# Performance work log

Hardware: AMD Instinct MI355X
Metric: run time of the kernel (lower is better)

The kernel has to match this reference:

```python
import jax, jax.numpy as jnp
import numpy as np

T, K = 131072, 128  # turns, num_tags


def setup_inputs() -> dict:
    key = jax.random.key(0)
    ks = jax.random.split(key, 8)
    emissions = jax.random.normal(ks[0], (T, K), dtype=jnp.float32)
    tags = jax.random.randint(ks[1], (T,), 0, K)
    who2who = jax.random.randint(ks[2], (T - 1,), 0, 2)
    init_count = jax.random.randint(ks[3], (T - 1,), 0, 2)
    distance = jax.random.randint(ks[4], (T - 1,), 0, 3)
    class_weights = jax.random.uniform(ks[5], (K,), jnp.float32, 0.5, 1.5)
    # DistanceCRF transition matrices stacked: [s2u, u2s_n0, u2s_n1_d2, u2s_n1_dgt2]
    trans_stack = jax.random.normal(ks[6], (4, K, K), dtype=jnp.float32) * 0.1
    start_scores = jax.random.normal(ks[7], (K,), dtype=jnp.float32) * 0.1
    return {
        "emissions": emissions,
        "trans_stack": trans_stack,
        "start_scores": start_scores,
        "class_weights": class_weights,
        "tags": tags,
        "who2who": who2who,
        "init_count": init_count,
        "distance": distance,
    }


def _trans_idx(who2who, init_count, distance):
    # DistanceCRF decision tree from _get_trans:
    #   w==1 -> s2u (0); init_count==0 -> u2s_n0 (1);
    #   distance==0 -> u2s_n1_d2 (2); else -> u2s_n1_dgt2 (3)
    return jnp.where(
        who2who == 1, 0,
        jnp.where(init_count == 0, 1, jnp.where(distance == 0, 2, 3)),
    )


def reference(emissions, trans_stack, start_scores, class_weights,
              tags, who2who, init_count, distance):
    idx = _trans_idx(who2who, init_count, distance)  # [T-1]

    # ---- gold path score (fully vectorized) ----
    w = class_weights[tags]                                   # [T]
    em_gold = jnp.take_along_axis(emissions, tags[:, None], axis=1)[:, 0]  # [T]
    tr_gold = trans_stack[idx, tags[:-1], tags[1:]]           # [T-1]
    gold = w[0] * (start_scores[tags[0]] + em_gold[0]) \
        + jnp.sum(w[1:] * (tr_gold + em_gold[1:]))

    # ---- forward algorithm (log partition) ----
    def step(alphas, xs):
        i, em_t = xs
        tr = trans_stack[i]                                   # [K,K] gathered per step
        scores = alphas[:, None] + tr + em_t[None, :]         # [K,K]
        return jax.nn.logsumexp(scores, axis=0), None

    alpha0 = start_scores + emissions[0]
    alphas, _ = jax.lax.scan(step, alpha0, (idx, emissions[1:]))
    log_Z = jax.nn.logsumexp(alphas)
    return gold, log_Z
```

## Files before the change

kernel.cpp:

```cpp
#include <hip/hip_runtime.h>

#define T_LEN 131072
#define KDIM 128
#define CHUNK 32
#define WARM 16
#define NSTEP (CHUNK + WARM)
#define NCHUNK (T_LEN / CHUNK)
#define GROUPC 16
#define NGRP (NCHUNK / GROUPC)
#define CSHIFT 4.5f

typedef float v4f __attribute__((ext_vector_type(4)));
typedef short s8v __attribute__((ext_vector_type(8)));

__device__ __forceinline__ int trans_idx(int w2w, int ic, int dist) {
    return (w2w == 1) ? 0 : (ic == 0 ? 1 : (dist == 0 ? 2 : 3));
}
__device__ __forceinline__ unsigned short bf16rne(float x) {
    unsigned u = __float_as_uint(x);
    return (unsigned short)((u + 0x7fffu + ((u >> 16) & 1u)) >> 16);
}
__device__ __forceinline__ float bf16tof(unsigned short h) {
    return __uint_as_float(((unsigned)h) << 16);
}

__global__ void __launch_bounds__(512, 1) scan_kernel(
    const float* __restrict__ em, const float* __restrict__ trans,
    const float* __restrict__ start, const float* __restrict__ cw,
    const int* __restrict__ tags, const int* __restrict__ w2w,
    const int* __restrict__ ic, const int* __restrict__ dist,
    double* __restrict__ goldslots, double* __restrict__ logzslots,
    unsigned* __restrict__ donecnt, float* __restrict__ out)
{
    const int tid = threadIdx.x;
    const int wv  = tid >> 6;
    const int mh  = wv >> 2;
    const int wvc = wv & 3;
    const int ln  = tid & 63;
    const int lr  = ln & 15;
    const int hq  = ln >> 4;
    const int grp = blockIdx.x;

    __shared__ float SS[32][130];
    __shared__ __align__(16) unsigned short A[2][GROUPC * KDIM];
    __shared__ double bg[8];
    __shared__ double bzred;
    __shared__ double redd[256];
    __shared__ int islast;

    s8v Bf[2][2][4];
    const int ncol = (wvc << 5) + lr;
    {
        const int sr = tid >> 4;
        const int sc = (tid & 15) << 3;
        float4 nx0, nx1;
        {
            const float* s = trans + (tid << 3);
            nx0 = *(const float4*)(s); nx1 = *(const float4*)(s + 4);
        }
        #pragma unroll
        for (int p = 0; p < 16; ++p) {
            ((float2*)&SS[sr][sc])[0] = make_float2(nx0.x, nx0.y);
            ((float2*)&SS[sr][sc])[1] = make_float2(nx0.z, nx0.w);
            ((float2*)&SS[sr][sc + 4])[0] = make_float2(nx1.x, nx1.y);
            ((float2*)&SS[sr][sc + 4])[1] = make_float2(nx1.z, nx1.w);
            __syncthreads();
            if (p < 15) {
                const float* s = trans + ((p + 1) << 12) + (tid << 3);
                nx0 = *(const float4*)(s); nx1 = *(const float4*)(s + 4);
            }
            if ((p >> 3) == mh) {
                const int mloc = (p >> 2) & 1, ks = p & 3;
                s8v f0, f1;
                #pragma unroll
                for (int j = 0; j < 8; ++j) {
                    f0[j] = (short)bf16rne(__expf(SS[(hq << 3) + j][ncol]));
                    f1[j] = (short)bf16rne(__expf(SS[(hq << 3) + j][ncol + 16]));
                }
                Bf[mloc][0][ks] = f0;
                Bf[mloc][1][ks] = f1;
            }
            __syncthreads();
        }
    }

    {
        float gp = 0.f;
        const int t = 1 + (grp << 9) + tid;
        if (t < T_LEN) {
            const int tg  = tags[t];
            const int tgp = tags[t - 1];
            const int mm  = trans_idx(w2w[t - 1], ic[t - 1], dist[t - 1]);
            gp = cw[tg] * (trans[((size_t)mm * KDIM + tgp) * KDIM + tg] +
                           em[(size_t)t * KDIM + tg]);
        }
        if (grp == 0 && tid == 0) {
            const int tg0 = tags[0];
            gp += cw[tg0] * (start[tg0] + em[tg0]);
        }
        float r = gp;
        #pragma unroll
        for (int off = 32; off; off >>= 1) r += __shfl_down(r, off, 64);
        if (ln == 0) bg[wv] = (double)r;
    }

    if (wv == 0) {
        const int c_row = (grp << 4) + lr;
        #pragma unroll
        for (int kk = 0; kk < 32; kk += 2) {
            const int k = (hq << 5) + kk;
            float a0, a1;
            if (c_row == 0) {
                a0 = __expf(start[k] + em[k]);
                a1 = __expf(start[k + 1] + em[k + 1]);
            } else { a0 = 1.f; a1 = 1.f; }
            const int off = (lr << 8) + ((k << 1) ^ ((lr & 7) << 4));
            *(unsigned*)((char*)A[0] + off) =
                (unsigned)bf16rne(a0) | ((unsigned)bf16rne(a1) << 16);
        }
    }
    __syncthreads();

    int t0r[4];
    #pragma unroll
    for (int r = 0; r < 4; ++r) {
        const int c_r = (grp << 4) + (hq << 2) + r;
        t0r[r] = (c_r == 0) ? 1 : (1 + c_r * CHUNK - WARM);
    }
    const int c_lr   = (grp << 4) + lr;
    const int town_l = 1 + c_lr * CHUNK;
    const int tend_l = min(town_l + CHUNK, T_LEN);
    const int t0_l   = (c_lr == 0) ? 1 : (town_l - WARM);

    int pmw, pmi, pmd;
    {
        const int ix = min(t0_l - 1, T_LEN - 2);
        pmw = w2w[ix]; pmi = ic[ix]; pmd = dist[ix];
    }
    float pem[2][4];
    #pragma unroll
    for (int r = 0; r < 4; ++r) {
        const int t = min(t0r[r], T_LEN - 1);
        pem[0][r] = em[(size_t)t * KDIM + ncol];
        pem[1][r] = em[(size_t)t * KDIM + ncol + 16];
    }

    float g = 0.f;
    float sc4[4] = {1.f, 1.f, 1.f, 1.f};

    for (int it = 0; it <= NSTEP; ++it) {
        s8v Af[4];
        #pragma unroll
        for (int ks = 0; ks < 4; ++ks) {
            const int off = (lr << 8) + (((ks << 6) + (hq << 4)) ^ ((lr & 7) << 4));
            Af[ks] = *(const s8v*)((const char*)A[it & 1] + off);
        }

        const bool trig = ((it & 7) == 0) || (grp == NGRP - 1 && it == NSTEP - 1);
        if (trig) {
            float s = 0.f;
            #pragma unroll
            for (int ks = 0; ks < 4; ++ks) {
                #pragma unroll
                for (int j = 0; j < 8; ++j)
                    s += bf16tof((unsigned short)Af[ks][j]);
            }
            s += __shfl_xor(s, 16, 64);
            s += __shfl_xor(s, 32, 64);
            const int tprev = t0_l + it - 1;
            const bool dn = ((tprev & 7) == 0) || (tprev == T_LEN - 1);
            const float scl = dn ? (1.f / s) : 1.f;
            if (it == 0) {
                if (c_lr == 0) g += __logf(s);
            } else if (dn && tprev >= town_l && tprev < tend_l) {
                g += __logf(s);
            }
            #pragma unroll
            for (int r = 0; r < 4; ++r) sc4[r] = __shfl(scl, (hq << 2) + r, 64);
        }
        if (it == NSTEP) break;

        const int mcur = trans_idx(pmw, pmi, pmd);
        int m4[4];
        #pragma unroll
        for (int r = 0; r < 4; ++r) m4[r] = __shfl(mcur, (hq << 2) + r, 64);
        float dv[2][4];
        #pragma unroll
        for (int nt = 0; nt < 2; ++nt) {
            #pragma unroll
            for (int r = 0; r < 4; ++r)
                dv[nt][r] = __expf(pem[nt][r] - CSHIFT) * sc4[r];
        }

        {
            const int ix = min(t0_l + it, T_LEN - 2);
            pmw = w2w[ix]; pmi = ic[ix]; pmd = dist[ix];
        }
        #pragma unroll
        for (int r = 0; r < 4; ++r) {
            const int t = min(t0r[r] + it + 1, T_LEN - 1);
            pem[0][r] = em[(size_t)t * KDIM + ncol];
            pem[1][r] = em[(size_t)t * KDIM + ncol + 16];
        }

        v4f acc[2][2];
        #pragma unroll
        for (int m = 0; m < 2; ++m) {
            #pragma unroll
            for (int nt = 0; nt < 2; ++nt) acc[m][nt] = (v4f)0.f;
        }
        #pragma unroll
        for (int ks = 0; ks < 4; ++ks) {
            #pragma unroll
            for (int m = 0; m < 2; ++m) {
                #pragma unroll
                for (int nt = 0; nt < 2; ++nt)
                    acc[m][nt] = __builtin_amdgcn_mfma_f32_16x16x32_bf16(
                        Af[ks], Bf[m][nt][ks], acc[m][nt], 0, 0, 0);
            }
        }

        #pragma unroll
        for (int nt = 0; nt < 2; ++nt) {
            #pragma unroll
            for (int r = 0; r < 4; ++r) {
                const int mm = m4[r];
                if ((mm >> 1) == mh) {
                    const float y = ((mm & 1) ? acc[1][nt][r] : acc[0][nt][r])
                                    * dv[nt][r];
                    const int row = (hq << 2) + r;
                    const int col = (wvc << 5) + (nt << 4) + lr;
                    const int off = (row << 8) + ((col << 1) ^ ((row & 7) << 4));
                    *(unsigned short*)((char*)A[(it & 1) ^ 1] + off) = bf16rne(y);
                }
            }
        }
        #pragma unroll
        for (int r = 0; r < 4; ++r) sc4[r] = 1.f;
        __syncthreads();
    }

    if (wv == 0) {
        float gz = (ln < 16) ? (g + CSHIFT * (float)(tend_l - town_l)) : 0.f;
        float r = gz;
        #pragma unroll
        for (int off = 32; off; off >>= 1) r += __shfl_down(r, off, 64);
        if (ln == 0) bzred = (double)r;
    }
    __syncthreads();

    if (tid == 0) {
        goldslots[grp] = bg[0] + bg[1] + bg[2] + bg[3] +
                         bg[4] + bg[5] + bg[6] + bg[7];
        logzslots[grp] = bzred;
        __threadfence();
        const unsigned prev = atomicAdd(donecnt, 1u);
        islast = (prev == NGRP - 1) ? 1 : 0;
    }
    __syncthreads();
    if (islast) {
        __threadfence();
        if (tid < 256) redd[tid] = goldslots[tid];
        __syncthreads();
        for (int s = 128; s > 0; s >>= 1) {
            if (tid < s && tid < 256) redd[tid] += redd[tid + s];
            __syncthreads();
        }
        if (tid == 0) out[0] = (float)redd[0];
        __syncthreads();
        if (tid < 256) redd[tid] = logzslots[tid];
        __syncthreads();
        for (int s = 128; s > 0; s >>= 1) {
            if (tid < s && tid < 256) redd[tid] += redd[tid + s];
            __syncthreads();
        }
        if (tid == 0) out[1] = (float)redd[0];
    }
}

extern "C" void kernel_launch(void* const* d_in, const int* in_sizes, int n_in,
                              void* d_out, int out_size, void* d_ws, size_t ws_size,
                              hipStream_t stream) {
    const float* emissions = (const float*)d_in[0];
    const float* trans     = (const float*)d_in[1];
    const float* start     = (const float*)d_in[2];
    const float* cw        = (const float*)d_in[3];
    const int*   tags      = (const int*)d_in[4];
    const int*   w2w       = (const int*)d_in[5];
    const int*   icnt      = (const int*)d_in[6];
    const int*   dist      = (const int*)d_in[7];

    double*   goldslots = (double*)d_ws;
    double*   logzslots = (double*)d_ws + 256;
    unsigned* donecnt   = (unsigned*)((double*)d_ws + 512);

    hipMemsetAsync(donecnt, 0, sizeof(unsigned), stream);
    scan_kernel<<<NGRP, 512, 0, stream>>>(emissions, trans, start, cw, tags,
                                          w2w, icnt, dist, goldslots, logzslots,
                                          donecnt, (float*)d_out);
}
```

Before: 170.7 us.

## Halve chunk length and double chunks per block with 1024-thread blocks

Cuts the per-chunk sequential scan from 32 to 16 owned steps, which shortens the serial critical path from 48 to 32 steps including warm-up. Each block now holds 32 chunks as two 16-row MFMA tiles using 16 waves, so the grid stays at 256 blocks. The per-step __syncthreads is replaced with an explicit lgkmcnt wait plus s_barrier. In exchange, warm-up work rises relative to useful work, 1024-thread blocks put more register pressure on each CU, and shorter warm-up chunks may be less accurate.

```diff
diff --git a/kernel.cpp b/kernel.cpp
--- a/kernel.cpp
+++ b/kernel.cpp
@@ -2,11 +2,11 @@
 
 #define T_LEN 131072
 #define KDIM 128
-#define CHUNK 32
+#define CHUNK 16
 #define WARM 16
 #define NSTEP (CHUNK + WARM)
 #define NCHUNK (T_LEN / CHUNK)
-#define GROUPC 16
+#define GROUPC 32
 #define NGRP (NCHUNK / GROUPC)
 #define CSHIFT 4.5f
 
@@ -24,7 +24,7 @@
     return __uint_as_float(((unsigned)h) << 16);
 }
 
-__global__ void __launch_bounds__(512, 1) scan_kernel(
+__global__ void __launch_bounds__(1024) scan_kernel(
     const float* __restrict__ em, const float* __restrict__ trans,
     const float* __restrict__ start, const float* __restrict__ cw,
     const int* __restrict__ tags, const int* __restrict__ w2w,
@@ -32,42 +32,37 @@
     double* __restrict__ goldslots, double* __restrict__ logzslots,
     unsigned* __restrict__ donecnt, float* __restrict__ out)
 {
-    const int tid = threadIdx.x;
-    const int wv  = tid >> 6;
-    const int mh  = wv >> 2;
-    const int wvc = wv & 3;
-    const int ln  = tid & 63;
-    const int lr  = ln & 15;
-    const int hq  = ln >> 4;
-    const int grp = blockIdx.x;
+    const int tid  = threadIdx.x;
+    const int wv   = tid >> 6;
+    const int mrow = wv >> 3;
+    const int mh   = (wv >> 2) & 1;
+    const int wvc  = wv & 3;
+    const int ln   = tid & 63;
+    const int lr   = ln & 15;
+    const int hq   = ln >> 4;
+    const int grp  = blockIdx.x;
 
     __shared__ float SS[32][130];
     __shared__ __align__(16) unsigned short A[2][GROUPC * KDIM];
-    __shared__ double bg[8];
-    __shared__ double bzred;
+    __shared__ double bg[16];
+    __shared__ double bzred[2];
     __shared__ double redd[256];
     __shared__ int islast;
 
     s8v Bf[2][2][4];
     const int ncol = (wvc << 5) + lr;
     {
-        const int sr = tid >> 4;
-        const int sc = (tid & 15) << 3;
-        float4 nx0, nx1;
-        {
-            const float* s = trans + (tid << 3);
-            nx0 = *(const float4*)(s); nx1 = *(const float4*)(s + 4);
-        }
+        const int sr = tid >> 5;
+        const int sc = (tid & 31) << 2;
+        float4 nx;
+        nx = *(const float4*)(trans + (tid << 2));
         #pragma unroll
         for (int p = 0; p < 16; ++p) {
-            ((float2*)&SS[sr][sc])[0] = make_float2(nx0.x, nx0.y);
-            ((float2*)&SS[sr][sc])[1] = make_float2(nx0.z, nx0.w);
-            ((float2*)&SS[sr][sc + 4])[0] = make_float2(nx1.x, nx1.y);
-            ((float2*)&SS[sr][sc + 4])[1] = make_float2(nx1.z, nx1.w);
+            ((float2*)&SS[sr][sc])[0] = make_float2(nx.x, nx.y);
+            ((float2*)&SS[sr][sc])[1] = make_float2(nx.z, nx.w);
             __syncthreads();
             if (p < 15) {
-                const float* s = trans + ((p + 1) << 12) + (tid << 3);
-                nx0 = *(const float4*)(s); nx1 = *(const float4*)(s + 4);
+                nx = *(const float4*)(trans + ((p + 1) << 12) + (tid << 2));
             }
             if ((p >> 3) == mh) {
                 const int mloc = (p >> 2) & 1, ks = p & 3;
@@ -86,13 +81,15 @@
 
     {
         float gp = 0.f;
-        const int t = 1 + (grp << 9) + tid;
-        if (t < T_LEN) {
-            const int tg  = tags[t];
-            const int tgp = tags[t - 1];
-            const int mm  = trans_idx(w2w[t - 1], ic[t - 1], dist[t - 1]);
-            gp = cw[tg] * (trans[((size_t)mm * KDIM + tgp) * KDIM + tg] +
-                           em[(size_t)t * KDIM + tg]);
+        if (tid < 512) {
+            const int t = 1 + (grp << 9) + tid;
+            if (t < T_LEN) {
+                const int tg  = tags[t];
+                const int tgp = tags[t - 1];
+                const int mm  = trans_idx(w2w[t - 1], ic[t - 1], dist[t - 1]);
+                gp = cw[tg] * (trans[((size_t)mm * KDIM + tgp) * KDIM + tg] +
+                               em[(size_t)t * KDIM + tg]);
+            }
         }
         if (grp == 0 && tid == 0) {
             const int tg0 = tags[0];
@@ -104,8 +101,9 @@
         if (ln == 0) bg[wv] = (double)r;
     }
 
-    if (wv == 0) {
-        const int c_row = (grp << 4) + lr;
+    if (mh == 0 && wvc == 0) {
+        const int rtile = (mrow << 4) + lr;
+        const int c_row = (grp << 5) + rtile;
         #pragma unroll
         for (int kk = 0; kk < 32; kk += 2) {
             const int k = (hq << 5) + kk;
@@ -114,7 +112,7 @@
                 a0 = __expf(start[k] + em[k]);
                 a1 = __expf(start[k + 1] + em[k + 1]);
             } else { a0 = 1.f; a1 = 1.f; }
-            const int off = (lr << 8) + ((k << 1) ^ ((lr & 7) << 4));
+            const int off = (rtile << 8) + ((k << 1) ^ ((lr & 7) << 4));
             *(unsigned*)((char*)A[0] + off) =
                 (unsigned)bf16rne(a0) | ((unsigned)bf16rne(a1) << 16);
         }
@@ -124,10 +122,10 @@
     int t0r[4];
     #pragma unroll
     for (int r = 0; r < 4; ++r) {
-        const int c_r = (grp << 4) + (hq << 2) + r;
+        const int c_r = (grp << 5) + (mrow << 4) + (hq << 2) + r;
         t0r[r] = (c_r == 0) ? 1 : (1 + c_r * CHUNK - WARM);
     }
-    const int c_lr   = (grp << 4) + lr;
+    const int c_lr   = (grp << 5) + (mrow << 4) + lr;
     const int town_l = 1 + c_lr * CHUNK;
     const int tend_l = min(town_l + CHUNK, T_LEN);
     const int t0_l   = (c_lr == 0) ? 1 : (town_l - WARM);
@@ -152,7 +150,8 @@
         s8v Af[4];
         #pragma unroll
         for (int ks = 0; ks < 4; ++ks) {
-            const int off = (lr << 8) + (((ks << 6) + (hq << 4)) ^ ((lr & 7) << 4));
+            const int off = (((mrow << 4) + lr) << 8)
+                          + (((ks << 6) + (hq << 4)) ^ ((lr & 7) << 4));
             Af[ks] = *(const s8v*)((const char*)A[it & 1] + off);
         }
 
@@ -228,31 +227,36 @@
                 if ((mm >> 1) == mh) {
                     const float y = ((mm & 1) ? acc[1][nt][r] : acc[0][nt][r])
                                     * dv[nt][r];
-                    const int row = (hq << 2) + r;
-                    const int col = (wvc << 5) + (nt << 4) + lr;
-                    const int off = (row << 8) + ((col << 1) ^ ((row & 7) << 4));
+                    const int rloc = (hq << 2) + r;
+                    const int row  = (mrow << 4) + rloc;
+                    const int col  = (wvc << 5) + (nt << 4) + lr;
+                    const int off  = (row << 8) + ((col << 1) ^ ((rloc & 7) << 4));
                     *(unsigned short*)((char*)A[(it & 1) ^ 1] + off) = bf16rne(y);
                 }
             }
         }
         #pragma unroll
         for (int r = 0; r < 4; ++r) sc4[r] = 1.f;
-        __syncthreads();
-    }
-
-    if (wv == 0) {
+
+        asm volatile("s_waitcnt lgkmcnt(0)" ::: "memory");
+        __builtin_amdgcn_s_barrier();
+    }
+
+    if (mh == 0 && wvc == 0) {
         float gz = (ln < 16) ? (g + CSHIFT * (float)(tend_l - town_l)) : 0.f;
         float r = gz;
         #pragma unroll
         for (int off = 32; off; off >>= 1) r += __shfl_down(r, off, 64);
-        if (ln == 0) bzred = (double)r;
+        if (ln == 0) bzred[mrow] = (double)r;
     }
     __syncthreads();
 
     if (tid == 0) {
-        goldslots[grp] = bg[0] + bg[1] + bg[2] + bg[3] +
-                         bg[4] + bg[5] + bg[6] + bg[7];
-        logzslots[grp] = bzred;
+        double G = 0.0;
+        #pragma unroll
+        for (int k = 0; k < 16; ++k) G += bg[k];
+        goldslots[grp] = G;
+        logzslots[grp] = bzred[0] + bzred[1];
         __threadfence();
         const unsigned prev = atomicAdd(donecnt, 1u);
         islast = (prev == NGRP - 1) ? 1 : 0;
@@ -263,7 +267,7 @@
         if (tid < 256) redd[tid] = goldslots[tid];
         __syncthreads();
         for (int s = 128; s > 0; s >>= 1) {
-            if (tid < s && tid < 256) redd[tid] += redd[tid + s];
+            if (tid < s) redd[tid] += redd[tid + s];
             __syncthreads();
         }
         if (tid == 0) out[0] = (float)redd[0];
@@ -271,7 +275,7 @@
         if (tid < 256) redd[tid] = logzslots[tid];
         __syncthreads();
         for (int s = 128; s > 0; s >>= 1) {
-            if (tid < s && tid < 256) redd[tid] += redd[tid + s];
+            if (tid < s) redd[tid] += redd[tid + s];
             __syncthreads();
         }
         if (tid == 0) out[1] = (float)redd[0];
@@ -295,7 +299,7 @@
     unsigned* donecnt   = (unsigned*)((double*)d_ws + 512);
 
     hipMemsetAsync(donecnt, 0, sizeof(unsigned), stream);
-    scan_kernel<<<NGRP, 512, 0, stream>>>(emissions, trans, start, cw, tags,
-                                          w2w, icnt, dist, goldslots, logzslots,
-                                          donecnt, (float*)d_out);
-}
+    scan_kernel<<<NGRP, 1024, 0, stream>>>(emissions, trans, start, cw, tags,
+                                           w2w, icnt, dist, goldslots, logzslots,
+                                           donecnt, (float*)d_out);
+}
```

Measured after the change: 309.1 us. 1.81x slower.
